# Kernel optimization log

Measured on AMD Instinct MI355X. Metric: run time of the kernel, lower is better.

Reference implementation:

```python
import jax, jax.numpy as jnp
import numpy as np

B, T, I, H, V = 128, 1024, 256, 512, 32000


def setup_inputs() -> dict:
    key = jax.random.key(0)
    ks = jax.random.split(key, 16)
    s = lambda fan_in: 1.0 / np.sqrt(fan_in)
    return {
        "x": jax.random.normal(ks[0], (B, 1, I), jnp.float32),
        "hp": jax.random.normal(ks[1], (1, B, H), jnp.float32),
        "cp": jax.random.normal(ks[2], (1, B, H), jnp.float32),
        "op": jax.random.normal(ks[3], (B, H), jnp.float32),
        "encoder_outputs": jax.random.normal(ks[4], (B, T, H), jnp.float32),
        # LSTM params (PyTorch gate order: i, f, g, o)
        "W_ih": jax.random.uniform(ks[5], (4 * H, I + H), jnp.float32, -s(H), s(H)),
        "W_hh": jax.random.uniform(ks[6], (4 * H, H), jnp.float32, -s(H), s(H)),
        "b_ih": jax.random.uniform(ks[7], (4 * H,), jnp.float32, -s(H), s(H)),
        "b_hh": jax.random.uniform(ks[8], (4 * H,), jnp.float32, -s(H), s(H)),
        # Bahdanau attention (all bias-free)
        "Wq": jax.random.uniform(ks[9], (H, H), jnp.float32, -s(H), s(H)),
        "Wm": jax.random.uniform(ks[10], (H, H), jnp.float32, -s(H), s(H)),
        "Wa": jax.random.uniform(ks[11], (1, H), jnp.float32, -s(H), s(H)),
        # output layers (bias-free)
        "Wo": jax.random.uniform(ks[12], (H, 2 * H), jnp.float32, -s(2 * H), s(2 * H)),
        "Wout": jax.random.uniform(ks[13], (V, H), jnp.float32, -s(H), s(H)),
    }


def reference(x, hp, cp, op, encoder_outputs, W_ih, W_hh, b_ih, b_hh, Wq, Wm, Wa, Wo, Wout):
    h = H  # hidden size
    # --- single-step LSTM (seq len 1) ---
    lstm_in = jnp.concatenate([x[:, 0, :], op], axis=-1)  # (B, I+H)
    gates = lstm_in @ W_ih.T + hp[0] @ W_hh.T + (b_ih + b_hh)  # (B, 4H)
    i_g = jax.nn.sigmoid(gates[:, 0 * h:1 * h])
    f_g = jax.nn.sigmoid(gates[:, 1 * h:2 * h])
    g_g = jnp.tanh(gates[:, 2 * h:3 * h])
    o_g = jax.nn.sigmoid(gates[:, 3 * h:4 * h])
    cn = f_g * cp[0] + i_g * g_g            # (B, H)
    hn = o_g * jnp.tanh(cn)                 # (B, H)

    # --- Bahdanau additive attention ---
    q = hn @ Wq.T                            # (B, H)
    k = jnp.einsum('bth,gh->btg', encoder_outputs, Wm)  # (B, T, H)
    scores = jnp.tanh(q[:, None, :] + k) @ Wa[0]         # (B, T)
    weights = jax.nn.softmax(scores, axis=1)             # softmax over time
    context = jnp.einsum('bt,btm->bm', weights, encoder_outputs)  # (B, H)

    # --- output head ---
    o_in = jnp.concatenate([hn, context], axis=1)  # (B, 2H)
    on = jnp.tanh(o_in @ Wo.T)                     # (B, H)
    output = jax.nn.log_softmax(on @ Wout.T, axis=1)  # (B, V)

    return (output, (hn[None], cn[None]), on, weights[:, None, :])
```

## Files before the change

### kernel.cpp

```cpp
#include <hip/hip_runtime.h>

#define B_ 128
#define T_ 1024
#define I_ 256
#define H_ 512
#define V_ 32000

typedef float  float4v __attribute__((ext_vector_type(4)));
typedef short  short8  __attribute__((ext_vector_type(8)));

__device__ __forceinline__ unsigned short f2bf(float f){
  unsigned int u = __float_as_uint(f);
  u += 0x7fffu + ((u >> 16) & 1u);
  return (unsigned short)(u >> 16);
}
__device__ __forceinline__ ushort4 f2bf4(float4 v){
  ushort4 u; u.x=f2bf(v.x); u.y=f2bf(v.y); u.z=f2bf(v.z); u.w=f2bf(v.w); return u;
}
__device__ __forceinline__ float fast_tanh(float x){
  float e = __expf(2.f*x);
  return 1.f - __fdividef(2.f, e + 1.f);
}
__device__ __forceinline__ float fast_sig(float x){
  return __fdividef(1.f, 1.f + __expf(-x));
}

__global__ void conv_bf16(const float4* __restrict__ src, ushort4* __restrict__ dst, int n4){
  int i = blockIdx.x*256 + threadIdx.x;
  if (i < n4) dst[i] = f2bf4(src[i]);
}

__device__ __forceinline__ const float* fetch_in(int mode, const float* a0, const float* a1,
                                                 const float* a2, int b, int k){
  if (mode == 0){
    if (k < 256)  return a0 + b*256 + k;
    if (k < 768)  return a1 + b*512 + (k-256);
    return a2 + b*512 + (k-768);
  }
  if (mode == 1) return a0 + b*512 + k;
  if (k < 512)   return a0 + b*512 + k;
  return a1 + b*512 + (k-512);
}
__device__ __forceinline__ const float* fetch_w(int mode, const float* w0, const float* w1,
                                                int n, int k){
  if (mode == 0){
    if (k < 768) return w0 + (size_t)n*768 + k;
    return w1 + (size_t)n*512 + (k-768);
  }
  if (mode == 1) return w0 + (size_t)n*512 + k;
  return w0 + (size_t)n*1024 + k;
}

__global__ void sgemm_acc(int mode,
    const float* __restrict__ a0, const float* __restrict__ a1, const float* __restrict__ a2,
    const float* __restrict__ w0, const float* __restrict__ w1,
    float* __restrict__ out, int N, int kchunk)
{
  __shared__ float inp_s[64*132];
  __shared__ float w_s[64*40];
  int tid = threadIdx.x;
  int nt = blockIdx.x, kid = blockIdx.y;
  int bg = tid & 31, ng = tid >> 5;
  int sb = tid >> 1, skof = (tid & 1)*32;
  int wn = tid & 31, wkg = tid >> 5;
  float acc[4][4] = {};
  int substeps = kchunk >> 6;

  for (int s = 0; s < substeps; ++s){
    int ks = kid*kchunk + s*64;
    __syncthreads();
    {
      const float* src = fetch_in(mode, a0, a1, a2, sb, ks + skof);
      #pragma unroll
      for (int j8 = 0; j8 < 8; ++j8){
        float4 v = ((const float4*)src)[j8];
        int kk = skof + j8*4;
        inp_s[(kk+0)*132 + sb] = v.x;
        inp_s[(kk+1)*132 + sb] = v.y;
        inp_s[(kk+2)*132 + sb] = v.z;
        inp_s[(kk+3)*132 + sb] = v.w;
      }
      int nglob = nt*32 + wn;
      const float* wsrc = fetch_w(mode, w0, w1, nglob, ks + wkg*8);
      float4 v0 = ((const float4*)wsrc)[0];
      float4 v1 = ((const float4*)wsrc)[1];
      int kk = wkg*8;
      w_s[(kk+0)*40 + wn] = v0.x;  w_s[(kk+1)*40 + wn] = v0.y;
      w_s[(kk+2)*40 + wn] = v0.z;  w_s[(kk+3)*40 + wn] = v0.w;
      w_s[(kk+4)*40 + wn] = v1.x;  w_s[(kk+5)*40 + wn] = v1.y;
      w_s[(kk+6)*40 + wn] = v1.z;  w_s[(kk+7)*40 + wn] = v1.w;
    }
    __syncthreads();
    #pragma unroll 4
    for (int k = 0; k < 64; ++k){
      float4v vb = *(const float4v*)&inp_s[k*132 + bg*4];
      float4v vw = *(const float4v*)&w_s[k*40 + ng*4];
      #pragma unroll
      for (int i = 0; i < 4; ++i)
        #pragma unroll
        for (int j = 0; j < 4; ++j)
          acc[i][j] = fmaf(vb[i], vw[j], acc[i][j]);
    }
  }
  #pragma unroll
  for (int i = 0; i < 4; ++i)
    #pragma unroll
    for (int j = 0; j < 4; ++j)
      atomicAdd(&out[(size_t)(bg*4+i)*N + nt*32 + ng*4 + j], acc[i][j]);
}

__global__ void lstm_act(const float* __restrict__ gates,
    const float* __restrict__ bih, const float* __restrict__ bhh,
    const float* __restrict__ cp, float* __restrict__ hn_out, float* __restrict__ cn_out)
{
  int i = blockIdx.x*256 + threadIdx.x;
  int b = i >> 9, h = i & 511;
  const float* g = gates + (size_t)b*2048;
  float g0 = g[h]      + bih[h]      + bhh[h];
  float g1 = g[512+h]  + bih[512+h]  + bhh[512+h];
  float g2 = g[1024+h] + bih[1024+h] + bhh[1024+h];
  float g3 = g[1536+h] + bih[1536+h] + bhh[1536+h];
  float ig = fast_sig(g0), fg = fast_sig(g1);
  float gg = fast_tanh(g2), og = fast_sig(g3);
  float cv = fg*cp[i] + ig*gg;
  float hv = og*fast_tanh(cv);
  cn_out[i] = cv;
  hn_out[i] = hv;
}

__global__ __launch_bounds__(1024) void attn_fused(
    const float* __restrict__ enc, const unsigned short* __restrict__ wmbf,
    const float* __restrict__ q, const float* __restrict__ wa,
    float* __restrict__ scores, float* __restrict__ ml, float* __restrict__ ctxp)
{
  __shared__ unsigned short As[128*40];
  __shared__ unsigned short Bs[512*40];
  __shared__ float qs[512], was[512], sbuf[128], ctxred[512], redbuf[4];

  int tid = threadIdx.x;
  int bidx = blockIdx.x >> 3, tc = blockIdx.x & 7;
  int tbase = tc * 128;
  int w = tid >> 6, lane = tid & 63;
  int wm = w >> 3, wn8 = w & 7;
  int c = lane & 15, q4 = lane >> 4;

  if (tid < 512){ qs[tid] = q[bidx*512 + tid]; was[tid] = wa[tid]; }
  if (tid < 128) sbuf[tid] = 0.f;

  float4v acc[4][4];
  #pragma unroll
  for (int i = 0; i < 4; ++i)
    #pragma unroll
    for (int j = 0; j < 4; ++j) acc[i][j] = (float4v)0.f;

  int arow = tid >> 3, akof = (tid & 7)*4;
  int brow = tid >> 1, bkof = (tid & 1)*16;
  const float* asrc = enc + ((size_t)bidx*1024 + tbase + arow)*512 + akof;
  const unsigned short* bsrc = wmbf + (size_t)brow*512 + bkof;

  for (int ks = 0; ks < 16; ++ks){
    int k0 = ks*32;
    __syncthreads();
    float4 va = *(const float4*)(asrc + k0);
    *(ushort4*)&As[arow*40 + akof] = f2bf4(va);
    const uint4* bp = (const uint4*)(bsrc + k0);
    uint4 b0 = bp[0], b1 = bp[1];
    *(uint4*)&Bs[brow*40 + bkof]     = b0;
    *(uint4*)&Bs[brow*40 + bkof + 8] = b1;
    __syncthreads();
    short8 af[4];
    #pragma unroll
    for (int mi = 0; mi < 4; ++mi)
      af[mi] = *(const short8*)&As[(wm*64 + mi*16 + c)*40 + q4*8];
    #pragma unroll
    for (int ni = 0; ni < 4; ++ni){
      short8 bf = *(const short8*)&Bs[(wn8*64 + ni*16 + c)*40 + q4*8];
      #pragma unroll
      for (int mi = 0; mi < 4; ++mi)
        acc[mi][ni] = __builtin_amdgcn_mfma_f32_16x16x32_bf16(af[mi], bf, acc[mi][ni], 0, 0, 0);
    }
  }
  __syncthreads();

  float qv[4], wv[4];
  #pragma unroll
  for (int ni = 0; ni < 4; ++ni){ int n = wn8*64 + ni*16 + c; qv[ni] = qs[n]; wv[ni] = was[n]; }
  #pragma unroll
  for (int mi = 0; mi < 4; ++mi){
    #pragma unroll
    for (int r = 0; r < 4; ++r){
      float v = 0.f;
      #pragma unroll
      for (int ni = 0; ni < 4; ++ni)
        v += wv[ni] * fast_tanh(qv[ni] + acc[mi][ni][r]);
      v += __shfl_xor(v, 1); v += __shfl_xor(v, 2);
      v += __shfl_xor(v, 4); v += __shfl_xor(v, 8);
      if (c == 0) atomicAdd(&sbuf[wm*64 + mi*16 + q4*4 + r], v);
    }
  }
  __syncthreads();

  float sval = 0.f;
  if (tid < 128){
    sval = sbuf[tid];
    scores[bidx*1024 + tbase + tid] = sval;
    float m = sval;
    m = fmaxf(m, __shfl_xor(m, 32)); m = fmaxf(m, __shfl_xor(m, 16));
    m = fmaxf(m, __shfl_xor(m, 8));  m = fmaxf(m, __shfl_xor(m, 4));
    m = fmaxf(m, __shfl_xor(m, 2));  m = fmaxf(m, __shfl_xor(m, 1));
    if (lane == 0) redbuf[w] = m;
  }
  __syncthreads();
  float mloc = fmaxf(redbuf[0], redbuf[1]);
  if (tid < 128){
    float p = __expf(sval - mloc);
    sbuf[tid] = p;
    float t = p;
    t += __shfl_xor(t, 32); t += __shfl_xor(t, 16); t += __shfl_xor(t, 8);
    t += __shfl_xor(t, 4);  t += __shfl_xor(t, 2);  t += __shfl_xor(t, 1);
    if (lane == 0) redbuf[2 + w] = t;
  }
  __syncthreads();
  if (tid == 0){
    ml[(bidx*8 + tc)*2 + 0] = mloc;
    ml[(bidx*8 + tc)*2 + 1] = redbuf[2] + redbuf[3];
  }
  int nn = tid & 511, tg = tid >> 9;
  const float* ep = enc + ((size_t)bidx*1024 + tbase + tg*64)*512 + nn;
  float a = 0.f;
  #pragma unroll 8
  for (int t2 = 0; t2 < 64; ++t2)
    a = fmaf(sbuf[tg*64 + t2], ep[(size_t)t2*512], a);
  if (tg == 1) ctxred[nn] = a;
  __syncthreads();
  if (tg == 0) ctxp[((size_t)bidx*8 + tc)*512 + nn] = a + ctxred[nn];
}

__global__ void attn_combine(const float* __restrict__ ml, const float* __restrict__ ctxp,
    const float* __restrict__ scores, float* __restrict__ ctx, float* __restrict__ wfinal)
{
  int b = blockIdx.x, tid = threadIdx.x;
  float M = -1e30f;
  #pragma unroll
  for (int i = 0; i < 8; ++i) M = fmaxf(M, ml[(b*8+i)*2]);
  float L = 0.f, ef[8];
  #pragma unroll
  for (int i = 0; i < 8; ++i){
    ef[i] = __expf(ml[(b*8+i)*2] - M);
    L += ml[(b*8+i)*2+1] * ef[i];
  }
  float invL = __fdividef(1.f, L);
  for (int n = tid; n < 512; n += 256){
    float v = 0.f;
    #pragma unroll
    for (int i = 0; i < 8; ++i) v += ef[i]*ctxp[((size_t)b*8 + i)*512 + n];
    ctx[b*512 + n] = v*invL;
  }
  for (int t = tid; t < 1024; t += 256)
    wfinal[b*1024 + t] = __expf(scores[b*1024 + t] - M)*invL;
}

__global__ void tanh_act(const float* __restrict__ in, float* __restrict__ out){
  int i = blockIdx.x*256 + threadIdx.x;
  out[i] = fast_tanh(in[i]);
}

__global__ void head_gemm(const float* __restrict__ onv, const float* __restrict__ wout,
                          float* __restrict__ outp)
{
  __shared__ unsigned short As[128*40];
  __shared__ unsigned short Bs[128*40];
  int tid = threadIdx.x;
  int n0 = blockIdx.x * 128;
  int w = tid >> 6, lane = tid & 63;
  int wm = w >> 1, wn = w & 1;
  int c = lane & 15, q4 = lane >> 4;
  float4v acc[4][4];
  #pragma unroll
  for (int i = 0; i < 4; ++i)
    #pragma unroll
    for (int j = 0; j < 4; ++j) acc[i][j] = (float4v)0.f;

  int row = tid >> 1, kof = (tid & 1)*16;
  const float* sa = onv + (size_t)row*512 + kof;
  const float* sb = wout + (size_t)(n0 + row)*512 + kof;

  for (int ks = 0; ks < 16; ++ks){
    int k0 = ks*32;
    __syncthreads();
    #pragma unroll
    for (int j = 0; j < 4; ++j){
      float4 va = *(const float4*)(sa + k0 + j*4);
      *(ushort4*)&As[row*40 + kof + j*4] = f2bf4(va);
      float4 vb = *(const float4*)(sb + k0 + j*4);
      *(ushort4*)&Bs[row*40 + kof + j*4] = f2bf4(vb);
    }
    __syncthreads();
    short8 af[4];
    #pragma unroll
    for (int mi = 0; mi < 4; ++mi)
      af[mi] = *(const short8*)&As[(wm*64 + mi*16 + c)*40 + q4*8];
    #pragma unroll
    for (int ni = 0; ni < 4; ++ni){
      short8 bf = *(const short8*)&Bs[(wn*64 + ni*16 + c)*40 + q4*8];
      #pragma unroll
      for (int mi = 0; mi < 4; ++mi)
        acc[mi][ni] = __builtin_amdgcn_mfma_f32_16x16x32_bf16(af[mi], bf, acc[mi][ni], 0, 0, 0);
    }
  }
  #pragma unroll
  for (int mi = 0; mi < 4; ++mi)
    #pragma unroll
    for (int ni = 0; ni < 4; ++ni)
      #pragma unroll
      for (int r = 0; r < 4; ++r){
        int m = wm*64 + mi*16 + q4*4 + r;
        int n = n0 + wn*64 + ni*16 + c;
        outp[(size_t)m*32000 + n] = acc[mi][ni][r];
      }
}

__global__ void lse_rows(const float* __restrict__ outp, float* __restrict__ lse){
  __shared__ float rm[4], rs[4];
  int b = blockIdx.x, tid = threadIdx.x;
  int w = tid >> 6, lane = tid & 63;
  const float* row = outp + (size_t)b*32000;
  float m = -1e30f, s = 0.f;
  for (int v = tid; v < 32000; v += 256){
    float x = row[v];
    if (x > m){ s = s*__expf(m - x) + 1.f; m = x; }
    else s += __expf(x - m);
  }
  for (int off = 32; off; off >>= 1){
    float mo = __shfl_xor(m, off), so = __shfl_xor(s, off);
    float M2 = fmaxf(m, mo);
    s = s*__expf(m - M2) + so*__expf(mo - M2);
    m = M2;
  }
  if (lane == 0){ rm[w] = m; rs[w] = s; }
  __syncthreads();
  if (tid == 0){
    float M2 = fmaxf(fmaxf(rm[0], rm[1]), fmaxf(rm[2], rm[3]));
    float S = rs[0]*__expf(rm[0]-M2) + rs[1]*__expf(rm[1]-M2)
            + rs[2]*__expf(rm[2]-M2) + rs[3]*__expf(rm[3]-M2);
    lse[b] = M2 + __logf(S);
  }
}

__global__ void sub_lse(float4* outp4, const float* __restrict__ lse){
  int i = blockIdx.x*256 + threadIdx.x;
  int b = i / 8000;
  float l = lse[b];
  float4 v = outp4[i];
  v.x -= l; v.y -= l; v.z -= l; v.w -= l;
  outp4[i] = v;
}

extern "C" void kernel_launch(void* const* d_in, const int* in_sizes, int n_in,
                              void* d_out, int out_size, void* d_ws, size_t ws_size,
                              hipStream_t stream)
{
  (void)in_sizes; (void)n_in; (void)out_size; (void)ws_size;
  const float* x    = (const float*)d_in[0];
  const float* hp   = (const float*)d_in[1];
  const float* cp   = (const float*)d_in[2];
  const float* op   = (const float*)d_in[3];
  const float* enc  = (const float*)d_in[4];
  const float* Wih  = (const float*)d_in[5];
  const float* Whh  = (const float*)d_in[6];
  const float* bih  = (const float*)d_in[7];
  const float* bhh  = (const float*)d_in[8];
  const float* Wq   = (const float*)d_in[9];
  const float* Wm   = (const float*)d_in[10];
  const float* Wa   = (const float*)d_in[11];
  const float* Wo   = (const float*)d_in[12];
  const float* Wout = (const float*)d_in[13];
  float* out = (float*)d_out;

  float* ws = (float*)d_ws;
  float* gates   = ws + 0;
  float* qbuf    = ws + 262144;
  unsigned short* wmbf = (unsigned short*)(ws + 327680);
  float* scoresb = ws + 458752;
  float* mlb     = ws + 589824;
  float* ctxpb   = ws + 591872;
  float* ctxb    = ws + 1116160;
  float* oaccb   = ws + 1181696;
  float* lseb    = ws + 1247232;

  float* out_logits = out;
  float* out_hn = out + 4096000;
  float* out_cn = out + 4161536;
  float* out_on = out + 4227072;
  float* out_w  = out + 4292608;

  hipMemsetAsync(gates, 0, (size_t)(262144 + 65536)*sizeof(float), stream);
  hipMemsetAsync(oaccb, 0, (size_t)65536*sizeof(float), stream);

  conv_bf16<<<256, 256, 0, stream>>>((const float4*)Wm, (ushort4*)wmbf, 65536);
  sgemm_acc<<<dim3(64, 4), 256, 0, stream>>>(0, x, op, hp, Wih, Whh, gates, 2048, 320);
  lstm_act<<<256, 256, 0, stream>>>(gates, bih, bhh, cp, out_hn, out_cn);
  sgemm_acc<<<dim3(16, 8), 256, 0, stream>>>(1, out_hn, nullptr, nullptr, Wq, nullptr, qbuf, 512, 64);
  attn_fused<<<1024, 1024, 0, stream>>>(enc, wmbf, qbuf, Wa, scoresb, mlb, ctxpb);
  attn_combine<<<128, 256, 0, stream>>>(mlb, ctxpb, scoresb, ctxb, out_w);
  sgemm_acc<<<dim3(16, 8), 256, 0, stream>>>(2, out_hn, ctxb, nullptr, Wo, nullptr, oaccb, 512, 128);
  tanh_act<<<256, 256, 0, stream>>>(oaccb, out_on);
  head_gemm<<<250, 256, 0, stream>>>(out_on, Wout, out_logits);
  lse_rows<<<128, 256, 0, stream>>>(out_logits, lseb);
  sub_lse<<<4000, 256, 0, stream>>>((float4*)out_logits, lseb);
}
```

Baseline: 772.9 us.

## Double-buffer attention GEMM tiles with register prefetch and halve block size

Restructures the fused attention kernel to use 512 threads with 8 waves, each computing a 64x128 tile, and double-buffers the LDS A/B tiles. Global loads for step k+2 are prefetched into registers while step k computes, which cuts the per-iteration barriers from two to one. The context reduction now has each thread sum all 128 timesteps, removing the cross-half LDS reduction. The larger accumulator tile (128 floats per lane) raises register pressure, and LDS use roughly doubles, which may limit the intended 2 blocks per CU.

```diff
diff --git a/kernel.cpp b/kernel.cpp
--- a/kernel.cpp
+++ b/kernel.cpp
@@ -128,70 +128,99 @@
   hn_out[i] = hv;
 }
 
-__global__ __launch_bounds__(1024) void attn_fused(
+__global__ __launch_bounds__(512, 2) void attn_fused(
     const float* __restrict__ enc, const unsigned short* __restrict__ wmbf,
     const float* __restrict__ q, const float* __restrict__ wa,
     float* __restrict__ scores, float* __restrict__ ml, float* __restrict__ ctxp)
 {
-  __shared__ unsigned short As[128*40];
-  __shared__ unsigned short Bs[512*40];
-  __shared__ float qs[512], was[512], sbuf[128], ctxred[512], redbuf[4];
+  __shared__ unsigned short As[2][128*40];
+  __shared__ unsigned short Bs[2][512*40];
+  __shared__ float qs[512], was[512], sbuf[128], redbuf[4];
 
   int tid = threadIdx.x;
   int bidx = blockIdx.x >> 3, tc = blockIdx.x & 7;
   int tbase = tc * 128;
   int w = tid >> 6, lane = tid & 63;
-  int wm = w >> 3, wn8 = w & 7;
+  int wm = w >> 2, wn4 = w & 3;
   int c = lane & 15, q4 = lane >> 4;
 
-  if (tid < 512){ qs[tid] = q[bidx*512 + tid]; was[tid] = wa[tid]; }
+  qs[tid]  = q[bidx*512 + tid];
+  was[tid] = wa[tid];
   if (tid < 128) sbuf[tid] = 0.f;
 
-  float4v acc[4][4];
+  float4v acc[4][8];
   #pragma unroll
   for (int i = 0; i < 4; ++i)
     #pragma unroll
-    for (int j = 0; j < 4; ++j) acc[i][j] = (float4v)0.f;
-
-  int arow = tid >> 3, akof = (tid & 7)*4;
-  int brow = tid >> 1, bkof = (tid & 1)*16;
+    for (int j = 0; j < 8; ++j) acc[i][j] = (float4v)0.f;
+
+  int arow = tid >> 2, akof = (tid & 3)*8;
   const float* asrc = enc + ((size_t)bidx*1024 + tbase + arow)*512 + akof;
-  const unsigned short* bsrc = wmbf + (size_t)brow*512 + bkof;
+  const unsigned short* bsrc = wmbf + (size_t)tid*512;
+
+  float4 pa0, pa1;
+  uint4  pb0, pb1, pb2, pb3;
+
+  pa0 = *(const float4*)(asrc);
+  pa1 = *(const float4*)(asrc + 4);
+  { const uint4* bp = (const uint4*)(bsrc);
+    pb0 = bp[0]; pb1 = bp[1]; pb2 = bp[2]; pb3 = bp[3]; }
+  {
+    unsigned short* asd = &As[0][arow*40 + akof];
+    *(ushort4*)asd       = f2bf4(pa0);
+    *(ushort4*)(asd + 4) = f2bf4(pa1);
+    uint4* bq = (uint4*)&Bs[0][tid*40];
+    bq[0] = pb0; bq[1] = pb1; bq[2] = pb2; bq[3] = pb3;
+  }
+  pa0 = *(const float4*)(asrc + 32);
+  pa1 = *(const float4*)(asrc + 36);
+  { const uint4* bp = (const uint4*)(bsrc + 32);
+    pb0 = bp[0]; pb1 = bp[1]; pb2 = bp[2]; pb3 = bp[3]; }
+  __syncthreads();
 
   for (int ks = 0; ks < 16; ++ks){
-    int k0 = ks*32;
-    __syncthreads();
-    float4 va = *(const float4*)(asrc + k0);
-    *(ushort4*)&As[arow*40 + akof] = f2bf4(va);
-    const uint4* bp = (const uint4*)(bsrc + k0);
-    uint4 b0 = bp[0], b1 = bp[1];
-    *(uint4*)&Bs[brow*40 + bkof]     = b0;
-    *(uint4*)&Bs[brow*40 + bkof + 8] = b1;
-    __syncthreads();
+    int cur = ks & 1;
+    if (ks < 15){
+      unsigned short* asd = &As[cur^1][arow*40 + akof];
+      *(ushort4*)asd       = f2bf4(pa0);
+      *(ushort4*)(asd + 4) = f2bf4(pa1);
+      uint4* bq = (uint4*)&Bs[cur^1][tid*40];
+      bq[0] = pb0; bq[1] = pb1; bq[2] = pb2; bq[3] = pb3;
+      if (ks < 14){
+        int k0 = (ks+2)*32;
+        pa0 = *(const float4*)(asrc + k0);
+        pa1 = *(const float4*)(asrc + k0 + 4);
+        const uint4* bp = (const uint4*)(bsrc + k0);
+        pb0 = bp[0]; pb1 = bp[1]; pb2 = bp[2]; pb3 = bp[3];
+      }
+    }
     short8 af[4];
     #pragma unroll
     for (int mi = 0; mi < 4; ++mi)
-      af[mi] = *(const short8*)&As[(wm*64 + mi*16 + c)*40 + q4*8];
-    #pragma unroll
-    for (int ni = 0; ni < 4; ++ni){
-      short8 bf = *(const short8*)&Bs[(wn8*64 + ni*16 + c)*40 + q4*8];
+      af[mi] = *(const short8*)&As[cur][(wm*64 + mi*16 + c)*40 + q4*8];
+    #pragma unroll
+    for (int ni = 0; ni < 8; ++ni){
+      short8 bf = *(const short8*)&Bs[cur][(wn4*128 + ni*16 + c)*40 + q4*8];
       #pragma unroll
       for (int mi = 0; mi < 4; ++mi)
         acc[mi][ni] = __builtin_amdgcn_mfma_f32_16x16x32_bf16(af[mi], bf, acc[mi][ni], 0, 0, 0);
     }
-  }
-  __syncthreads();
-
-  float qv[4], wv[4];
-  #pragma unroll
-  for (int ni = 0; ni < 4; ++ni){ int n = wn8*64 + ni*16 + c; qv[ni] = qs[n]; wv[ni] = was[n]; }
+    __syncthreads();
+  }
+
+  float qv[8], wv[8];
+  #pragma unroll
+  for (int ni = 0; ni < 8; ++ni){
+    int n = wn4*128 + ni*16 + c;
+    qv[ni] = qs[n]; wv[ni] = was[n];
+  }
   #pragma unroll
   for (int mi = 0; mi < 4; ++mi){
     #pragma unroll
     for (int r = 0; r < 4; ++r){
       float v = 0.f;
       #pragma unroll
-      for (int ni = 0; ni < 4; ++ni)
+      for (int ni = 0; ni < 8; ++ni)
         v += wv[ni] * fast_tanh(qv[ni] + acc[mi][ni][r]);
       v += __shfl_xor(v, 1); v += __shfl_xor(v, 2);
       v += __shfl_xor(v, 4); v += __shfl_xor(v, 8);
@@ -225,15 +254,12 @@
     ml[(bidx*8 + tc)*2 + 0] = mloc;
     ml[(bidx*8 + tc)*2 + 1] = redbuf[2] + redbuf[3];
   }
-  int nn = tid & 511, tg = tid >> 9;
-  const float* ep = enc + ((size_t)bidx*1024 + tbase + tg*64)*512 + nn;
+  const float* ep = enc + ((size_t)bidx*1024 + tbase)*512 + tid;
   float a = 0.f;
   #pragma unroll 8
-  for (int t2 = 0; t2 < 64; ++t2)
-    a = fmaf(sbuf[tg*64 + t2], ep[(size_t)t2*512], a);
-  if (tg == 1) ctxred[nn] = a;
-  __syncthreads();
-  if (tg == 0) ctxp[((size_t)bidx*8 + tc)*512 + nn] = a + ctxred[nn];
+  for (int t2 = 0; t2 < 128; ++t2)
+    a = fmaf(sbuf[t2], ep[(size_t)t2*512], a);
+  ctxp[((size_t)bidx*8 + tc)*512 + tid] = a;
 }
 
 __global__ void attn_combine(const float* __restrict__ ml, const float* __restrict__ ctxp,
@@ -401,7 +427,7 @@
   sgemm_acc<<<dim3(64, 4), 256, 0, stream>>>(0, x, op, hp, Wih, Whh, gates, 2048, 320);
   lstm_act<<<256, 256, 0, stream>>>(gates, bih, bhh, cp, out_hn, out_cn);
   sgemm_acc<<<dim3(16, 8), 256, 0, stream>>>(1, out_hn, nullptr, nullptr, Wq, nullptr, qbuf, 512, 64);
-  attn_fused<<<1024, 1024, 0, stream>>>(enc, wmbf, qbuf, Wa, scoresb, mlb, ctxpb);
+  attn_fused<<<1024, 512, 0, stream>>>(enc, wmbf, qbuf, Wa, scoresb, mlb, ctxpb);
   attn_combine<<<128, 256, 0, stream>>>(mlb, ctxpb, scoresb, ctxb, out_w);
   sgemm_acc<<<dim3(16, 8), 256, 0, stream>>>(2, out_hn, ctxb, nullptr, Wo, nullptr, oaccb, 512, 128);
   tanh_act<<<256, 256, 0, stream>>>(oaccb, out_on);
```

After: 751.8 us. 1.03x faster.

## Split attention into tiled score GEMM, softmax, and context kernels with double buffering

Applied to the files above, without the earlier changes.

Replaces the monolithic 1024-thread attention kernel with three kernels. The score GEMM uses 128x128 tiles over the hidden dimension in 256-thread blocks, with double-buffered XOR-swizzled LDS, register prefetch and packed bf16 conversion. It writes per-N-chunk partial scores. A separate softmax kernel reduces these, and a context kernel rereads the encoder outputs and accumulates with atomics. This raises occupancy and overlaps loads with MFMA, at the cost of one extra full pass over the 256MB encoder tensor and four times the A-tile conversion work.

```diff
diff --git a/kernel.cpp b/kernel.cpp
--- a/kernel.cpp
+++ b/kernel.cpp
@@ -16,6 +16,11 @@
 }
 __device__ __forceinline__ ushort4 f2bf4(float4 v){
   ushort4 u; u.x=f2bf(v.x); u.y=f2bf(v.y); u.z=f2bf(v.z); u.w=f2bf(v.w); return u;
+}
+__device__ __forceinline__ unsigned int cvt_pk_bf16(float lo, float hi){
+  unsigned int r;
+  asm volatile("v_cvt_pk_bf16_f32 %0, %1, %2" : "=v"(r) : "v"(lo), "v"(hi));
+  return r;
 }
 __device__ __forceinline__ float fast_tanh(float x){
   float e = __expf(2.f*x);
@@ -128,63 +133,105 @@
   hn_out[i] = hv;
 }
 
-__global__ __launch_bounds__(1024) void attn_fused(
+__global__ __launch_bounds__(256, 4) void attn_gemm(
     const float* __restrict__ enc, const unsigned short* __restrict__ wmbf,
     const float* __restrict__ q, const float* __restrict__ wa,
-    float* __restrict__ scores, float* __restrict__ ml, float* __restrict__ ctxp)
-{
-  __shared__ unsigned short As[128*40];
-  __shared__ unsigned short Bs[512*40];
-  __shared__ float qs[512], was[512], sbuf[128], ctxred[512], redbuf[4];
+    float* __restrict__ sp)
+{
+  __shared__ unsigned short As[2][4096];
+  __shared__ unsigned short Bs[2][4096];
+  __shared__ float sred[2][128];
 
   int tid = threadIdx.x;
-  int bidx = blockIdx.x >> 3, tc = blockIdx.x & 7;
-  int tbase = tc * 128;
+  int blk = blockIdx.x;
+  int nc = blk & 3, tc = (blk >> 2) & 7, b = blk >> 5;
+  int tbase = tc*128, n0 = nc*128;
   int w = tid >> 6, lane = tid & 63;
-  int wm = w >> 3, wn8 = w & 7;
+  int wm = w >> 1, wn = w & 1;
   int c = lane & 15, q4 = lane >> 4;
 
-  if (tid < 512){ qs[tid] = q[bidx*512 + tid]; was[tid] = wa[tid]; }
-  if (tid < 128) sbuf[tid] = 0.f;
-
   float4v acc[4][4];
   #pragma unroll
   for (int i = 0; i < 4; ++i)
     #pragma unroll
     for (int j = 0; j < 4; ++j) acc[i][j] = (float4v)0.f;
 
-  int arow = tid >> 3, akof = (tid & 7)*4;
-  int brow = tid >> 1, bkof = (tid & 1)*16;
-  const float* asrc = enc + ((size_t)bidx*1024 + tbase + arow)*512 + akof;
-  const unsigned short* bsrc = wmbf + (size_t)brow*512 + bkof;
+  int sr = tid >> 1, sh = tid & 1;
+  const float* asrc = enc + ((size_t)(b*1024 + tbase + sr))*512 + sh*16;
+  const unsigned short* bsrc = wmbf + (size_t)(n0 + sr)*512 + sh*16;
+  int srp = sr >> 1, sodd = sr & 1;
+  int wo0 = srp*64 + ((sodd*4 + sh*2    ) ^ (srp & 7))*8;
+  int wo1 = srp*64 + ((sodd*4 + sh*2 + 1) ^ (srp & 7))*8;
+
+  int a_off[4], b_off[4];
+  #pragma unroll
+  for (int mi = 0; mi < 4; ++mi){
+    int r = wm*64 + mi*16 + c;
+    a_off[mi] = (r >> 1)*64 + (((r & 1)*4 + q4) ^ ((r >> 1) & 7))*8;
+  }
+  #pragma unroll
+  for (int ni = 0; ni < 4; ++ni){
+    int r = wn*64 + ni*16 + c;
+    b_off[ni] = (r >> 1)*64 + (((r & 1)*4 + q4) ^ ((r >> 1) & 7))*8;
+  }
+
+  float4 a0, a1, a2, a3;
+  uint4 bv0, bv1;
+
+  a0 = ((const float4*)asrc)[0]; a1 = ((const float4*)asrc)[1];
+  a2 = ((const float4*)asrc)[2]; a3 = ((const float4*)asrc)[3];
+  bv0 = *(const uint4*)(bsrc);   bv1 = *(const uint4*)(bsrc + 8);
+  {
+    uint4 ca, cb;
+    ca.x = cvt_pk_bf16(a0.x, a0.y); ca.y = cvt_pk_bf16(a0.z, a0.w);
+    ca.z = cvt_pk_bf16(a1.x, a1.y); ca.w = cvt_pk_bf16(a1.z, a1.w);
+    cb.x = cvt_pk_bf16(a2.x, a2.y); cb.y = cvt_pk_bf16(a2.z, a2.w);
+    cb.z = cvt_pk_bf16(a3.x, a3.y); cb.w = cvt_pk_bf16(a3.z, a3.w);
+    *(uint4*)&As[0][wo0] = ca; *(uint4*)&As[0][wo1] = cb;
+    *(uint4*)&Bs[0][wo0] = bv0; *(uint4*)&Bs[0][wo1] = bv1;
+  }
+  a0 = ((const float4*)(asrc + 32))[0]; a1 = ((const float4*)(asrc + 32))[1];
+  a2 = ((const float4*)(asrc + 32))[2]; a3 = ((const float4*)(asrc + 32))[3];
+  bv0 = *(const uint4*)(bsrc + 32);     bv1 = *(const uint4*)(bsrc + 40);
+  __syncthreads();
 
   for (int ks = 0; ks < 16; ++ks){
-    int k0 = ks*32;
-    __syncthreads();
-    float4 va = *(const float4*)(asrc + k0);
-    *(ushort4*)&As[arow*40 + akof] = f2bf4(va);
-    const uint4* bp = (const uint4*)(bsrc + k0);
-    uint4 b0 = bp[0], b1 = bp[1];
-    *(uint4*)&Bs[brow*40 + bkof]     = b0;
-    *(uint4*)&Bs[brow*40 + bkof + 8] = b1;
-    __syncthreads();
+    int cur = ks & 1;
+    if (ks < 15){
+      uint4 ca, cb;
+      ca.x = cvt_pk_bf16(a0.x, a0.y); ca.y = cvt_pk_bf16(a0.z, a0.w);
+      ca.z = cvt_pk_bf16(a1.x, a1.y); ca.w = cvt_pk_bf16(a1.z, a1.w);
+      cb.x = cvt_pk_bf16(a2.x, a2.y); cb.y = cvt_pk_bf16(a2.z, a2.w);
+      cb.z = cvt_pk_bf16(a3.x, a3.y); cb.w = cvt_pk_bf16(a3.z, a3.w);
+      *(uint4*)&As[cur^1][wo0] = ca; *(uint4*)&As[cur^1][wo1] = cb;
+      *(uint4*)&Bs[cur^1][wo0] = bv0; *(uint4*)&Bs[cur^1][wo1] = bv1;
+      if (ks < 14){
+        int k0 = (ks + 2)*32;
+        a0 = ((const float4*)(asrc + k0))[0]; a1 = ((const float4*)(asrc + k0))[1];
+        a2 = ((const float4*)(asrc + k0))[2]; a3 = ((const float4*)(asrc + k0))[3];
+        bv0 = *(const uint4*)(bsrc + k0);     bv1 = *(const uint4*)(bsrc + k0 + 8);
+      }
+    }
     short8 af[4];
     #pragma unroll
     for (int mi = 0; mi < 4; ++mi)
-      af[mi] = *(const short8*)&As[(wm*64 + mi*16 + c)*40 + q4*8];
+      af[mi] = *(const short8*)&As[cur][a_off[mi]];
     #pragma unroll
     for (int ni = 0; ni < 4; ++ni){
-      short8 bf = *(const short8*)&Bs[(wn8*64 + ni*16 + c)*40 + q4*8];
+      short8 bf = *(const short8*)&Bs[cur][b_off[ni]];
       #pragma unroll
       for (int mi = 0; mi < 4; ++mi)
         acc[mi][ni] = __builtin_amdgcn_mfma_f32_16x16x32_bf16(af[mi], bf, acc[mi][ni], 0, 0, 0);
     }
-  }
-  __syncthreads();
+    __syncthreads();
+  }
 
   float qv[4], wv[4];
   #pragma unroll
-  for (int ni = 0; ni < 4; ++ni){ int n = wn8*64 + ni*16 + c; qv[ni] = qs[n]; wv[ni] = was[n]; }
+  for (int ni = 0; ni < 4; ++ni){
+    int n = n0 + wn*64 + ni*16 + c;
+    qv[ni] = q[b*512 + n]; wv[ni] = wa[n];
+  }
   #pragma unroll
   for (int mi = 0; mi < 4; ++mi){
     #pragma unroll
@@ -195,69 +242,59 @@
         v += wv[ni] * fast_tanh(qv[ni] + acc[mi][ni][r]);
       v += __shfl_xor(v, 1); v += __shfl_xor(v, 2);
       v += __shfl_xor(v, 4); v += __shfl_xor(v, 8);
-      if (c == 0) atomicAdd(&sbuf[wm*64 + mi*16 + q4*4 + r], v);
-    }
-  }
-  __syncthreads();
-
-  float sval = 0.f;
-  if (tid < 128){
-    sval = sbuf[tid];
-    scores[bidx*1024 + tbase + tid] = sval;
-    float m = sval;
-    m = fmaxf(m, __shfl_xor(m, 32)); m = fmaxf(m, __shfl_xor(m, 16));
-    m = fmaxf(m, __shfl_xor(m, 8));  m = fmaxf(m, __shfl_xor(m, 4));
-    m = fmaxf(m, __shfl_xor(m, 2));  m = fmaxf(m, __shfl_xor(m, 1));
-    if (lane == 0) redbuf[w] = m;
-  }
-  __syncthreads();
-  float mloc = fmaxf(redbuf[0], redbuf[1]);
-  if (tid < 128){
-    float p = __expf(sval - mloc);
-    sbuf[tid] = p;
-    float t = p;
-    t += __shfl_xor(t, 32); t += __shfl_xor(t, 16); t += __shfl_xor(t, 8);
-    t += __shfl_xor(t, 4);  t += __shfl_xor(t, 2);  t += __shfl_xor(t, 1);
-    if (lane == 0) redbuf[2 + w] = t;
-  }
-  __syncthreads();
-  if (tid == 0){
-    ml[(bidx*8 + tc)*2 + 0] = mloc;
-    ml[(bidx*8 + tc)*2 + 1] = redbuf[2] + redbuf[3];
-  }
-  int nn = tid & 511, tg = tid >> 9;
-  const float* ep = enc + ((size_t)bidx*1024 + tbase + tg*64)*512 + nn;
+      if (c == 0) sred[wn][wm*64 + mi*16 + q4*4 + r] = v;
+    }
+  }
+  __syncthreads();
+  if (tid < 128)
+    sp[nc*131072 + b*1024 + tbase + tid] = sred[0][tid] + sred[1][tid];
+}
+
+__global__ __launch_bounds__(1024) void attn_softmax(const float* __restrict__ sp,
+                                                     float* __restrict__ wf)
+{
+  __shared__ float red[16];
+  int b = blockIdx.x, tid = threadIdx.x;
+  int w = tid >> 6, lane = tid & 63;
+  float s = sp[b*1024 + tid] + sp[131072 + b*1024 + tid]
+          + sp[262144 + b*1024 + tid] + sp[393216 + b*1024 + tid];
+  float m = s;
+  m = fmaxf(m, __shfl_xor(m, 32)); m = fmaxf(m, __shfl_xor(m, 16));
+  m = fmaxf(m, __shfl_xor(m, 8));  m = fmaxf(m, __shfl_xor(m, 4));
+  m = fmaxf(m, __shfl_xor(m, 2));  m = fmaxf(m, __shfl_xor(m, 1));
+  if (lane == 0) red[w] = m;
+  __syncthreads();
+  float M = red[0];
+  #pragma unroll
+  for (int i = 1; i < 16; ++i) M = fmaxf(M, red[i]);
+  __syncthreads();
+  float p = __expf(s - M);
+  float t = p;
+  t += __shfl_xor(t, 32); t += __shfl_xor(t, 16); t += __shfl_xor(t, 8);
+  t += __shfl_xor(t, 4);  t += __shfl_xor(t, 2);  t += __shfl_xor(t, 1);
+  if (lane == 0) red[w] = t;
+  __syncthreads();
+  float L = 0.f;
+  #pragma unroll
+  for (int i = 0; i < 16; ++i) L += red[i];
+  wf[b*1024 + tid] = p * __fdividef(1.f, L);
+}
+
+__global__ __launch_bounds__(512) void attn_ctx(const float* __restrict__ wgt,
+    const float* __restrict__ enc, float* __restrict__ ctx)
+{
+  __shared__ float wl[128];
+  int blk = blockIdx.x;
+  int b = blk >> 3, tc = blk & 7;
+  int tid = threadIdx.x;
+  if (tid < 128) wl[tid] = wgt[b*1024 + tc*128 + tid];
+  __syncthreads();
+  const float* ep = enc + ((size_t)(b*1024 + tc*128))*512 + tid;
   float a = 0.f;
   #pragma unroll 8
-  for (int t2 = 0; t2 < 64; ++t2)
-    a = fmaf(sbuf[tg*64 + t2], ep[(size_t)t2*512], a);
-  if (tg == 1) ctxred[nn] = a;
-  __syncthreads();
-  if (tg == 0) ctxp[((size_t)bidx*8 + tc)*512 + nn] = a + ctxred[nn];
-}
-
-__global__ void attn_combine(const float* __restrict__ ml, const float* __restrict__ ctxp,
-    const float* __restrict__ scores, float* __restrict__ ctx, float* __restrict__ wfinal)
-{
-  int b = blockIdx.x, tid = threadIdx.x;
-  float M = -1e30f;
-  #pragma unroll
-  for (int i = 0; i < 8; ++i) M = fmaxf(M, ml[(b*8+i)*2]);
-  float L = 0.f, ef[8];
-  #pragma unroll
-  for (int i = 0; i < 8; ++i){
-    ef[i] = __expf(ml[(b*8+i)*2] - M);
-    L += ml[(b*8+i)*2+1] * ef[i];
-  }
-  float invL = __fdividef(1.f, L);
-  for (int n = tid; n < 512; n += 256){
-    float v = 0.f;
-    #pragma unroll
-    for (int i = 0; i < 8; ++i) v += ef[i]*ctxp[((size_t)b*8 + i)*512 + n];
-    ctx[b*512 + n] = v*invL;
-  }
-  for (int t = tid; t < 1024; t += 256)
-    wfinal[b*1024 + t] = __expf(scores[b*1024 + t] - M)*invL;
+  for (int t2 = 0; t2 < 128; ++t2)
+    a = fmaf(wl[t2], ep[(size_t)t2*512], a);
+  atomicAdd(&ctx[b*512 + tid], a);
 }
 
 __global__ void tanh_act(const float* __restrict__ in, float* __restrict__ out){
@@ -381,12 +418,10 @@
   float* gates   = ws + 0;
   float* qbuf    = ws + 262144;
   unsigned short* wmbf = (unsigned short*)(ws + 327680);
-  float* scoresb = ws + 458752;
-  float* mlb     = ws + 589824;
-  float* ctxpb   = ws + 591872;
-  float* ctxb    = ws + 1116160;
-  float* oaccb   = ws + 1181696;
-  float* lseb    = ws + 1247232;
+  float* spb     = ws + 458752;
+  float* ctxb    = ws + 983040;
+  float* oaccb   = ws + 1048576;
+  float* lseb    = ws + 1114112;
 
   float* out_logits = out;
   float* out_hn = out + 4096000;
@@ -395,14 +430,15 @@
   float* out_w  = out + 4292608;
 
   hipMemsetAsync(gates, 0, (size_t)(262144 + 65536)*sizeof(float), stream);
-  hipMemsetAsync(oaccb, 0, (size_t)65536*sizeof(float), stream);
+  hipMemsetAsync(ctxb, 0, (size_t)(65536 + 65536)*sizeof(float), stream);
 
   conv_bf16<<<256, 256, 0, stream>>>((const float4*)Wm, (ushort4*)wmbf, 65536);
   sgemm_acc<<<dim3(64, 4), 256, 0, stream>>>(0, x, op, hp, Wih, Whh, gates, 2048, 320);
   lstm_act<<<256, 256, 0, stream>>>(gates, bih, bhh, cp, out_hn, out_cn);
   sgemm_acc<<<dim3(16, 8), 256, 0, stream>>>(1, out_hn, nullptr, nullptr, Wq, nullptr, qbuf, 512, 64);
-  attn_fused<<<1024, 1024, 0, stream>>>(enc, wmbf, qbuf, Wa, scoresb, mlb, ctxpb);
-  attn_combine<<<128, 256, 0, stream>>>(mlb, ctxpb, scoresb, ctxb, out_w);
+  attn_gemm<<<4096, 256, 0, stream>>>(enc, wmbf, qbuf, Wa, spb);
+  attn_softmax<<<128, 1024, 0, stream>>>(spb, out_w);
+  attn_ctx<<<1024, 512, 0, stream>>>(out_w, enc, ctxb);
   sgemm_acc<<<dim3(16, 8), 256, 0, stream>>>(2, out_hn, ctxb, nullptr, Wo, nullptr, oaccb, 512, 128);
   tanh_act<<<256, 256, 0, stream>>>(oaccb, out_on);
   head_gemm<<<250, 256, 0, stream>>>(out_on, Wout, out_logits);
```

Measured after the change: 771.4 us. Within noise of the previous version (-0.2%).
